# Kernel optimization log

Measured on AMD Instinct MI355X. Metric: run time of the kernel, lower is better.

The kernel has to match this reference:

```python
import jax, jax.numpy as jnp
import numpy as np

EPS = 1e-5
N_HEAD = 8
N_FREQS = 65
EMB_DIM = 128
E_DIM = 4            # ceil(256 / 65)
V_DIM = EMB_DIM // N_HEAD
CTX = 10


def prelu(x, a):
    return jnp.where(x >= 0, x, a * x)


def ln_last(x, g, b):
    # LayerNormalization4DCF_new: normalize over the fused (freq, chan) last axis
    mu = jnp.mean(x, axis=-1, keepdims=True)
    var = jnp.mean((x - mu) ** 2, axis=-1, keepdims=True)
    return (x - mu) / jnp.sqrt(var + EPS) * g + b


def head_proj(x, W, b, a, g, bt, H, Dh):
    # x: [B, T, F, C] -> [B*H, T, F*Dh], LayerNorm over last dim
    B, T, F, C = x.shape
    y = prelu(jnp.einsum('btfc,oc->btfo', x, W) + b, a)
    y = y.reshape(B, T, F, H, Dh).transpose(0, 3, 1, 2, 4).reshape(B * H, T, F * Dh)
    return ln_last(y, g, bt)


def setup_inputs() -> dict:
    key = jax.random.key(0)
    ks = jax.random.split(key, 8)
    B, T = 4, 500
    d = {}
    d['x'] = jax.random.normal(ks[0], (B, EMB_DIM, N_FREQS, T), dtype=jnp.float32)
    d['merged_context'] = jax.random.normal(ks[1], (B, EMB_DIM, N_FREQS, T), dtype=jnp.float32)
    d['K_buf'] = jnp.zeros((B * N_HEAD, CTX - 1, N_FREQS * E_DIM), dtype=jnp.float32)
    d['V_buf'] = jnp.zeros((B * N_HEAD, CTX - 1, N_FREQS * V_DIM), dtype=jnp.float32)
    d['W_Q'] = jax.random.normal(ks[2], (E_DIM * N_HEAD, EMB_DIM), dtype=jnp.float32) * 0.05
    d['b_Q'] = jnp.zeros((E_DIM * N_HEAD,), dtype=jnp.float32)
    d['a_Q'] = jnp.full((1,), 0.25, dtype=jnp.float32)
    d['g_Q'] = jnp.ones((N_FREQS * E_DIM,), dtype=jnp.float32)
    d['be_Q'] = jnp.zeros((N_FREQS * E_DIM,), dtype=jnp.float32)
    d['W_K'] = jax.random.normal(ks[3], (E_DIM * N_HEAD, EMB_DIM), dtype=jnp.float32) * 0.05
    d['b_K'] = jnp.zeros((E_DIM * N_HEAD,), dtype=jnp.float32)
    d['a_K'] = jnp.full((1,), 0.25, dtype=jnp.float32)
    d['g_K'] = jnp.ones((N_FREQS * E_DIM,), dtype=jnp.float32)
    d['be_K'] = jnp.zeros((N_FREQS * E_DIM,), dtype=jnp.float32)
    d['W_V'] = jax.random.normal(ks[4], (EMB_DIM, EMB_DIM), dtype=jnp.float32) * 0.05
    d['b_V'] = jnp.zeros((EMB_DIM,), dtype=jnp.float32)
    d['a_V'] = jnp.full((1,), 0.25, dtype=jnp.float32)
    d['g_V'] = jnp.ones((N_FREQS * V_DIM,), dtype=jnp.float32)
    d['be_V'] = jnp.zeros((N_FREQS * V_DIM,), dtype=jnp.float32)
    d['W_P'] = jax.random.normal(ks[5], (EMB_DIM, EMB_DIM), dtype=jnp.float32) * 0.05
    d['b_P'] = jnp.zeros((EMB_DIM,), dtype=jnp.float32)
    d['a_P'] = jnp.full((1,), 0.25, dtype=jnp.float32)
    d['g_P'] = jnp.ones((N_FREQS * EMB_DIM,), dtype=jnp.float32)
    d['be_P'] = jnp.zeros((N_FREQS * EMB_DIM,), dtype=jnp.float32)
    return d


def reference(x, merged_context, K_buf, V_buf,
              W_Q, b_Q, a_Q, g_Q, be_Q,
              W_K, b_K, a_K, g_K, be_K,
              W_V, b_V, a_V, g_V, be_V,
              W_P, b_P, a_P, g_P, be_P):
    # x, merged_context: [B, C, F, T] -> [B, T, F, C]
    xp = jnp.transpose(x, (0, 3, 2, 1))
    mc = jnp.transpose(merged_context, (0, 3, 2, 1))
    B, T, F, C = xp.shape
    H = N_HEAD

    Q = head_proj(xp, W_Q, b_Q, a_Q, g_Q, be_Q, H, E_DIM)     # [B*H, T, F*E]
    K = head_proj(mc, W_K, b_K, a_K, g_K, be_K, H, V_DIM * 0 + E_DIM)
    V = head_proj(mc, W_V, b_V, a_V, g_V, be_V, H, V_DIM)     # [B*H, T, F*Vd]

    Kfull = jnp.concatenate([K_buf, K], axis=1)               # [B*H, T+ctx-1, F*E]
    Vfull = jnp.concatenate([V_buf, V], axis=1)               # [B*H, T+ctx-1, F*Vd]
    K_buf_new = Kfull[:, -(CTX - 1):]
    V_buf_new = Vfull[:, -(CTX - 1):]

    # causal sliding windows of length ctx: [B*H, T, ctx, D]
    idx = jnp.arange(T)[:, None] + jnp.arange(CTX)[None, :]
    Kw = Kfull[:, idx, :]
    Vw = Vfull[:, idx, :]

    dqk = F * E_DIM
    scores = jnp.einsum('btd,btcd->btc', Q, Kw) / jnp.sqrt(jnp.float32(dqk))
    p = jax.nn.softmax(scores, axis=-1)                        # [B*H, T, ctx]
    Vo = jnp.einsum('btc,btcd->btd', p, Vw)                    # [B*H, T, F*Vd]

    # reassemble channels: [B*H, T, F*Vd] -> [B, T, F, H*Vd]
    z = Vo.reshape(B, H, T, F, V_DIM).transpose(0, 2, 3, 1, 4).reshape(B, T, F, H * V_DIM)

    y = prelu(jnp.einsum('btfc,oc->btfo', z, W_P) + b_P, a_P)  # [B, T, F, C]
    y = ln_last(y.reshape(B, T, F * C), g_P, be_P).reshape(B, T, F, C)

    out = y + xp
    out = jnp.transpose(out, (0, 3, 2, 1))                     # [B, C, F, T]
    return out, K_buf_new, V_buf_new
```

## Files before the change

### kernel.cpp

```cpp
#include <hip/hip_runtime.h>
#include <math.h>

#define NB   4
#define NT   500
#define NF   65
#define NC   128
#define NH   8
#define NE   4
#define NV   16
#define NCTX 10
#define DQ   260
#define DV   1040
#define DP   8320

#define MQ 0
#define RQ 16000
#define MK 32000
#define RK 48000
#define MV 64000
#define RV 80000

__global__ __launch_bounds__(256, 4) void proj32_k(const float* __restrict__ x,
    const float* __restrict__ W, const float* __restrict__ bias,
    const float* __restrict__ a, float* __restrict__ out,
    float* __restrict__ sS, float* __restrict__ sS2)
{
    __shared__ float Wl[NC * 32];
    int b = blockIdx.x / NF, f = blockIdx.x % NF;
    for (int idx = threadIdx.x; idx < 32 * NC; idx += 256) {
        int o = idx & 31, c = idx >> 5;
        Wl[c * 32 + o] = W[o * NC + c];
    }
    __syncthreads();
    int og = threadIdx.x >> 6;
    int tg = threadIdx.x & 63;
    int t0 = blockIdx.y * 256 + tg * 4;
    int t0c = t0 <= NT - 4 ? t0 : NT - 4;
    const float* xp = x + ((size_t)(b * NC) * NF + f) * NT + t0c;
    const float* wp = Wl + og * 8;
    const size_t xs = (size_t)NF * NT;
    float4 acc[8];
#pragma unroll
    for (int i = 0; i < 8; i++) acc[i] = make_float4(0.f, 0.f, 0.f, 0.f);
#pragma unroll 4
    for (int c = 0; c < NC; c++) {
        float4 xv = *(const float4*)(xp + (size_t)c * xs);
        const float* wc = wp + c * 32;
        float wv[8];
        *(float4*)(wv)     = *(const float4*)(wc);
        *(float4*)(wv + 4) = *(const float4*)(wc + 4);
#pragma unroll
        for (int i = 0; i < 8; i++) {
            acc[i].x += xv.x * wv[i];
            acc[i].y += xv.y * wv[i];
            acc[i].z += xv.z * wv[i];
            acc[i].w += xv.w * wv[i];
        }
    }
    if (t0 > NT - 4) return;
    float av = a[0];
#pragma unroll
    for (int i = 0; i < 8; i++) {
        int o = og * 8 + i;
        float bo = bias[o];
        float4 v = acc[i];
        v.x += bo; v.y += bo; v.z += bo; v.w += bo;
        v.x = v.x >= 0.f ? v.x : av * v.x;
        v.y = v.y >= 0.f ? v.y : av * v.y;
        v.z = v.z >= 0.f ? v.z : av * v.z;
        v.w = v.w >= 0.f ? v.w : av * v.w;
        acc[i] = v;
        int h = o >> 2, e = o & 3;
        *(float4*)(out + ((size_t)(b * NH + h) * DQ + f * NE + e) * NT + t0) = v;
    }
#pragma unroll
    for (int hh = 0; hh < 2; hh++) {
        int h = og * 2 + hh;
        float s0 = 0.f, s1 = 0.f, s2 = 0.f, s3 = 0.f;
        float q0 = 0.f, q1 = 0.f, q2 = 0.f, q3 = 0.f;
#pragma unroll
        for (int e = 0; e < 4; e++) {
            float4 v = acc[hh * 4 + e];
            s0 += v.x; s1 += v.y; s2 += v.z; s3 += v.w;
            q0 += v.x * v.x; q1 += v.y * v.y; q2 += v.z * v.z; q3 += v.w * v.w;
        }
        int base = (b * NH + h) * NT + t0;
        atomicAdd(&sS[base],     s0); atomicAdd(&sS[base + 1], s1);
        atomicAdd(&sS[base + 2], s2); atomicAdd(&sS[base + 3], s3);
        atomicAdd(&sS2[base],     q0); atomicAdd(&sS2[base + 1], q1);
        atomicAdd(&sS2[base + 2], q2); atomicAdd(&sS2[base + 3], q3);
    }
}

__global__ __launch_bounds__(256, 4) void projV_k(const float* __restrict__ x,
    const float* __restrict__ W, const float* __restrict__ bias,
    const float* __restrict__ a, float* __restrict__ out,
    float* __restrict__ sS, float* __restrict__ sS2)
{
    __shared__ float Wl[NC * 64];
    int b = blockIdx.x / NF, f = blockIdx.x % NF;
    int o0 = blockIdx.z * 64;
    for (int idx = threadIdx.x; idx < 64 * NC; idx += 256) {
        int o = idx & 63, c = idx >> 6;
        Wl[c * 64 + o] = W[(o0 + o) * NC + c];
    }
    __syncthreads();
    int og = threadIdx.x >> 6;
    int tg = threadIdx.x & 63;
    int t0 = blockIdx.y * 256 + tg * 4;
    int t0c = t0 <= NT - 4 ? t0 : NT - 4;
    const float* xp = x + ((size_t)(b * NC) * NF + f) * NT + t0c;
    const float* wp = Wl + og * 16;
    const size_t xs = (size_t)NF * NT;
    float4 acc[16];
#pragma unroll
    for (int i = 0; i < 16; i++) acc[i] = make_float4(0.f, 0.f, 0.f, 0.f);
#pragma unroll 2
    for (int c = 0; c < NC; c++) {
        float4 xv = *(const float4*)(xp + (size_t)c * xs);
        const float* wc = wp + c * 64;
        float wv[16];
        *(float4*)(wv)      = *(const float4*)(wc);
        *(float4*)(wv + 4)  = *(const float4*)(wc + 4);
        *(float4*)(wv + 8)  = *(const float4*)(wc + 8);
        *(float4*)(wv + 12) = *(const float4*)(wc + 12);
#pragma unroll
        for (int i = 0; i < 16; i++) {
            acc[i].x += xv.x * wv[i];
            acc[i].y += xv.y * wv[i];
            acc[i].z += xv.z * wv[i];
            acc[i].w += xv.w * wv[i];
        }
    }
    if (t0 > NT - 4) return;
    float av = a[0];
    int h = (o0 >> 4) + og;
    float s0 = 0.f, s1 = 0.f, s2 = 0.f, s3 = 0.f;
    float q0 = 0.f, q1 = 0.f, q2 = 0.f, q3 = 0.f;
#pragma unroll
    for (int i = 0; i < 16; i++) {
        int o = o0 + og * 16 + i;
        float bo = bias[o];
        float4 v = acc[i];
        v.x += bo; v.y += bo; v.z += bo; v.w += bo;
        v.x = v.x >= 0.f ? v.x : av * v.x;
        v.y = v.y >= 0.f ? v.y : av * v.y;
        v.z = v.z >= 0.f ? v.z : av * v.z;
        v.w = v.w >= 0.f ? v.w : av * v.w;
        *(float4*)(out + ((size_t)(b * NH + h) * DV + f * NV + i) * NT + t0) = v;
        s0 += v.x; s1 += v.y; s2 += v.z; s3 += v.w;
        q0 += v.x * v.x; q1 += v.y * v.y; q2 += v.z * v.z; q3 += v.w * v.w;
    }
    int base = (b * NH + h) * NT + t0;
    atomicAdd(&sS[base],     s0); atomicAdd(&sS[base + 1], s1);
    atomicAdd(&sS[base + 2], s2); atomicAdd(&sS[base + 3], s3);
    atomicAdd(&sS2[base],     q0); atomicAdd(&sS2[base + 1], q1);
    atomicAdd(&sS2[base + 2], q2); atomicAdd(&sS2[base + 3], q3);
}

__global__ __launch_bounds__(256, 4) void projP_k(const float* __restrict__ VoT,
    const float* __restrict__ W, const float* __restrict__ bias,
    const float* __restrict__ a, float* __restrict__ yraw,
    float* __restrict__ sP, float* __restrict__ s2P)
{
    __shared__ float Wl[NC * 64];
    int b = blockIdx.x / NF, f = blockIdx.x % NF;
    int o0 = blockIdx.z * 64;
    for (int idx = threadIdx.x; idx < 64 * NC; idx += 256) {
        int o = idx & 63, c = idx >> 6;
        Wl[c * 64 + o] = W[(o0 + o) * NC + c];
    }
    __syncthreads();
    int og = threadIdx.x >> 6;
    int tg = threadIdx.x & 63;
    int t0 = blockIdx.y * 256 + tg * 4;
    int t0c = t0 <= NT - 4 ? t0 : NT - 4;
    const float* zp = VoT + ((size_t)(b * NH) * DV + f * NV) * NT + t0c;
    const float* wp = Wl + og * 16;
    float4 acc[16];
#pragma unroll
    for (int i = 0; i < 16; i++) acc[i] = make_float4(0.f, 0.f, 0.f, 0.f);
    for (int hc = 0; hc < NH; hc++) {
        const float* zh = zp + (size_t)hc * DV * NT;
        const float* wh = wp + hc * 16 * 64;
#pragma unroll
        for (int v = 0; v < NV; v++) {
            float4 xv = *(const float4*)(zh + (size_t)v * NT);
            const float* wc = wh + v * 64;
            float wv[16];
            *(float4*)(wv)      = *(const float4*)(wc);
            *(float4*)(wv + 4)  = *(const float4*)(wc + 4);
            *(float4*)(wv + 8)  = *(const float4*)(wc + 8);
            *(float4*)(wv + 12) = *(const float4*)(wc + 12);
#pragma unroll
            for (int i = 0; i < 16; i++) {
                acc[i].x += xv.x * wv[i];
                acc[i].y += xv.y * wv[i];
                acc[i].z += xv.z * wv[i];
                acc[i].w += xv.w * wv[i];
            }
        }
    }
    if (t0 > NT - 4) return;
    float av = a[0];
    float s0 = 0.f, s1 = 0.f, s2 = 0.f, s3 = 0.f;
    float q0 = 0.f, q1 = 0.f, q2 = 0.f, q3 = 0.f;
#pragma unroll
    for (int i = 0; i < 16; i++) {
        int o = o0 + og * 16 + i;
        float bo = bias[o];
        float4 v = acc[i];
        v.x += bo; v.y += bo; v.z += bo; v.w += bo;
        v.x = v.x >= 0.f ? v.x : av * v.x;
        v.y = v.y >= 0.f ? v.y : av * v.y;
        v.z = v.z >= 0.f ? v.z : av * v.z;
        v.w = v.w >= 0.f ? v.w : av * v.w;
        *(float4*)(yraw + ((size_t)(b * NC + o) * NF + f) * NT + t0) = v;
        s0 += v.x; s1 += v.y; s2 += v.z; s3 += v.w;
        q0 += v.x * v.x; q1 += v.y * v.y; q2 += v.z * v.z; q3 += v.w * v.w;
    }
    int base = b * NT + t0;
    atomicAdd(&sP[base],     s0); atomicAdd(&sP[base + 1], s1);
    atomicAdd(&sP[base + 2], s2); atomicAdd(&sP[base + 3], s3);
    atomicAdd(&s2P[base],     q0); atomicAdd(&s2P[base + 1], q1);
    atomicAdd(&s2P[base + 2], q2); atomicAdd(&s2P[base + 3], q3);
}

__global__ __launch_bounds__(256) void finqkv_k(const float* __restrict__ stats,
    float* __restrict__ murs)
{
    int i = blockIdx.x * 256 + threadIdx.x;
    if (i >= 48000) return;
    int seg = i / 16000, j = i % 16000;
    float S = stats[seg * 32000 + j], S2 = stats[seg * 32000 + 16000 + j];
    float D = (seg < 2) ? 260.f : 1040.f;
    float mu = S / D;
    float var = S2 / D - mu * mu;
    murs[seg * 32000 + j] = mu;
    murs[seg * 32000 + 16000 + j] = rsqrtf(var + 1e-5f);
}

__global__ __launch_bounds__(256) void finp_k(const float* __restrict__ sP,
    const float* __restrict__ s2P, float* __restrict__ muP, float* __restrict__ rsP)
{
    int i = blockIdx.x * 256 + threadIdx.x;
    if (i >= NB * NT) return;
    float inv = 1.0f / (float)DP;
    float mu = sP[i] * inv;
    float var = s2P[i] * inv - mu * mu;
    muP[i] = mu;
    rsP[i] = rsqrtf(var + 1e-5f);
}

__global__ void copybuf_k(const float* __restrict__ Kt, const float* __restrict__ Vt,
    const float* __restrict__ murs,
    const float* __restrict__ g_K, const float* __restrict__ be_K,
    const float* __restrict__ g_V, const float* __restrict__ be_V,
    float* __restrict__ outK, float* __restrict__ outV)
{
    int i = blockIdx.x * 256 + threadIdx.x;
    const int NK = 32 * 9 * DQ;
    const int NVb = 32 * 9 * DV;
    if (i < NK) {
        int bh = i / (9 * DQ); int r = i % (9 * DQ); int j = r / DQ; int d = r % DQ;
        int tt = 491 + j;
        float v = Kt[(size_t)(bh * DQ + d) * NT + tt];
        float mu = murs[MK + bh * NT + tt], rs = murs[RK + bh * NT + tt];
        outK[i] = (v - mu) * rs * g_K[d] + be_K[d];
    } else if (i < NK + NVb) {
        int i2 = i - NK;
        int bh = i2 / (9 * DV); int r = i2 % (9 * DV); int j = r / DV; int d = r % DV;
        int tt = 491 + j;
        float v = Vt[(size_t)(bh * DV + d) * NT + tt];
        float mu = murs[MV + bh * NT + tt], rs = murs[RV + bh * NT + tt];
        outV[i2] = (v - mu) * rs * g_V[d] + be_V[d];
    }
}

__global__ __launch_bounds__(128) void scores_s1_k(const float* __restrict__ Qt,
    const float* __restrict__ Kt, const float* __restrict__ Kbuf,
    const float* __restrict__ murs,
    const float* __restrict__ g_Q, const float* __restrict__ be_Q,
    const float* __restrict__ g_K, const float* __restrict__ be_K,
    float* __restrict__ spart)
{
    int bh = blockIdx.x;
    int t = blockIdx.y * 128 + threadIdx.x;
    if (t >= NT) return;
    int z = blockIdx.z;
    int d0 = z * 13;
    float rsq = murs[RQ + bh * NT + t];
    float mq = -murs[MQ + bh * NT + t] * rsq;
    float s[NCTX];
    if (t >= NCTX - 1) {
        float rkc[NCTX], mkc[NCTX];
#pragma unroll
        for (int c = 0; c < NCTX; c++) {
            int tk = t - (NCTX - 1) + c;
            rkc[c] = murs[RK + bh * NT + tk];
            mkc[c] = -murs[MK + bh * NT + tk] * rkc[c];
        }
        float A[NCTX], SG = 0.f, SB = 0.f;
#pragma unroll
        for (int c = 0; c < NCTX; c++) A[c] = 0.f;
        const float* qp = Qt + ((size_t)bh * DQ + d0) * NT + t;
        const float* kp = Kt + ((size_t)bh * DQ + d0) * NT + (t - (NCTX - 1));
#pragma unroll 4
        for (int d = 0; d < 13; d++) {
            float gq = g_Q[d0 + d], bq = be_Q[d0 + d];
            float gk = g_K[d0 + d], bk = be_K[d0 + d];
            float qln = (qp[(size_t)d * NT] * rsq + mq) * gq + bq;
            float qg = qln * gk;
            SG += qg; SB += qln * bk;
            const float* kr = kp + (size_t)d * NT;
#pragma unroll
            for (int c = 0; c < NCTX; c++) A[c] += qg * kr[c];
        }
#pragma unroll
        for (int c = 0; c < NCTX; c++) s[c] = rkc[c] * A[c] + mkc[c] * SG + SB;
    } else {
#pragma unroll
        for (int c = 0; c < NCTX; c++) s[c] = 0.f;
        for (int d = 0; d < 13; d++) {
            float gq = g_Q[d0 + d], bq = be_Q[d0 + d];
            float gk = g_K[d0 + d], bk = be_K[d0 + d];
            float qln = (Qt[((size_t)bh * DQ + d0 + d) * NT + t] * rsq + mq) * gq + bq;
#pragma unroll
            for (int c = 0; c < NCTX; c++) {
                int tc = t + c;
                float kv;
                if (tc < NCTX - 1) {
                    kv = Kbuf[((size_t)bh * (NCTX - 1) + tc) * DQ + d0 + d];
                } else {
                    int tk = tc - (NCTX - 1);
                    float rk = murs[RK + bh * NT + tk];
                    float mk = murs[MK + bh * NT + tk];
                    kv = (Kt[((size_t)bh * DQ + d0 + d) * NT + tk] - mk) * rk * gk + bk;
                }
                s[c] += qln * kv;
            }
        }
    }
#pragma unroll
    for (int c = 0; c < NCTX; c++)
        spart[(size_t)((z * 32 + bh) * NCTX + c) * NT + t] = s[c];
}

__global__ __launch_bounds__(128) void softmax_k(const float* __restrict__ spart,
    float* __restrict__ p)
{
    int bh = blockIdx.x;
    int t = blockIdx.y * 128 + threadIdx.x;
    if (t >= NT) return;
    float s[NCTX];
#pragma unroll
    for (int c = 0; c < NCTX; c++) s[c] = 0.f;
    for (int z = 0; z < 20; z++) {
#pragma unroll
        for (int c = 0; c < NCTX; c++)
            s[c] += spart[(size_t)((z * 32 + bh) * NCTX + c) * NT + t];
    }
    const float sc = 0.06201736729460423f;
    float m = -1e30f;
#pragma unroll
    for (int c = 0; c < NCTX; c++) { s[c] *= sc; m = fmaxf(m, s[c]); }
    float den = 0.f;
#pragma unroll
    for (int c = 0; c < NCTX; c++) { s[c] = __expf(s[c] - m); den += s[c]; }
    float iden = 1.0f / den;
#pragma unroll
    for (int c = 0; c < NCTX; c++) p[(size_t)(bh * NCTX + c) * NT + t] = s[c] * iden;
}

__global__ __launch_bounds__(128) void vo_k(const float* __restrict__ p,
    const float* __restrict__ Vt, const float* __restrict__ Vbuf,
    const float* __restrict__ murs,
    const float* __restrict__ g_V, const float* __restrict__ be_V,
    float* __restrict__ VoT)
{
    int bh = blockIdx.x;
    int t = blockIdx.y * 128 + threadIdx.x;
    if (t >= NT) return;
    int d0 = blockIdx.z * 16;
    float pc[NCTX];
#pragma unroll
    for (int c = 0; c < NCTX; c++) pc[c] = p[(size_t)(bh * NCTX + c) * NT + t];
    if (t >= NCTX - 1) {
        float prs[NCTX], Cm = 0.f, Cp = 0.f;
#pragma unroll
        for (int c = 0; c < NCTX; c++) {
            int tv = t - (NCTX - 1) + c;
            float rs = murs[RV + bh * NT + tv];
            prs[c] = pc[c] * rs;
            Cm += pc[c] * (-murs[MV + bh * NT + tv] * rs);
            Cp += pc[c];
        }
        const float* vp = Vt + ((size_t)bh * DV + d0) * NT + (t - (NCTX - 1));
        float* op = VoT + ((size_t)bh * DV + d0) * NT + t;
#pragma unroll 4
        for (int d = 0; d < 16; d++) {
            float gv = g_V[d0 + d], bv = be_V[d0 + d];
            const float* vr = vp + (size_t)d * NT;
            float A = 0.f;
#pragma unroll
            for (int c = 0; c < NCTX; c++) A += prs[c] * vr[c];
            op[(size_t)d * NT] = gv * (A + Cm) + bv * Cp;
        }
    } else {
        for (int d = 0; d < 16; d++) {
            float gv = g_V[d0 + d], bv = be_V[d0 + d];
            float acc = 0.f;
#pragma unroll
            for (int c = 0; c < NCTX; c++) {
                int tc = t + c;
                float v;
                if (tc < NCTX - 1) {
                    v = Vbuf[((size_t)bh * (NCTX - 1) + tc) * DV + d0 + d];
                } else {
                    int tv = tc - (NCTX - 1);
                    float rs = murs[RV + bh * NT + tv];
                    float mu = murs[MV + bh * NT + tv];
                    v = (Vt[((size_t)bh * DV + d0 + d) * NT + tv] - mu) * rs * gv + bv;
                }
                acc += pc[c] * v;
            }
            VoT[((size_t)bh * DV + d0 + d) * NT + t] = acc;
        }
    }
}

__global__ __launch_bounds__(256) void lnp_apply(const float* __restrict__ yraw,
    const float* __restrict__ x, const float* __restrict__ g, const float* __restrict__ be,
    const float* __restrict__ muA, const float* __restrict__ rstdA, float* __restrict__ out)
{
    int bo = blockIdx.x; int b = bo >> 7, o = bo & 127;
    int t = blockIdx.y * 256 + threadIdx.x;
    if (t >= NT) return;
    float mu = muA[b * NT + t], rstd = rstdA[b * NT + t];
    for (int f = 0; f < NF; f++) {
        size_t idx = (size_t)((b * NC + o) * NF + f) * NT + t;
        int i = f * NC + o;
        float v = yraw[idx];
        out[idx] = (v - mu) * rstd * g[i] + be[i] + x[idx];
    }
}

extern "C" void kernel_launch(void* const* d_in, const int* in_sizes, int n_in,
                              void* d_out, int out_size, void* d_ws, size_t ws_size,
                              hipStream_t stream) {
    const float* x    = (const float*)d_in[0];
    const float* mc   = (const float*)d_in[1];
    const float* Kbuf = (const float*)d_in[2];
    const float* Vbuf = (const float*)d_in[3];
    const float* W_Q  = (const float*)d_in[4];
    const float* b_Q  = (const float*)d_in[5];
    const float* a_Q  = (const float*)d_in[6];
    const float* g_Q  = (const float*)d_in[7];
    const float* be_Q = (const float*)d_in[8];
    const float* W_K  = (const float*)d_in[9];
    const float* b_K  = (const float*)d_in[10];
    const float* a_K  = (const float*)d_in[11];
    const float* g_K  = (const float*)d_in[12];
    const float* be_K = (const float*)d_in[13];
    const float* W_V  = (const float*)d_in[14];
    const float* b_V  = (const float*)d_in[15];
    const float* a_V  = (const float*)d_in[16];
    const float* g_V  = (const float*)d_in[17];
    const float* be_V = (const float*)d_in[18];
    const float* W_P  = (const float*)d_in[19];
    const float* b_P  = (const float*)d_in[20];
    const float* a_P  = (const float*)d_in[21];
    const float* g_P  = (const float*)d_in[22];
    const float* be_P = (const float*)d_in[23];

    float* out  = (float*)d_out;
    float* outK = out + (size_t)NB * NC * NF * NT;
    float* outV = outK + 32 * 9 * DQ;

    float* stats = out;
    float* murs  = out + 96000;

    float* ws = (float*)d_ws;
    float* Qt   = ws;
    float* Kt   = Qt + (size_t)32 * DQ * NT;
    float* Vt   = Kt + (size_t)32 * DQ * NT;
    float* VoT  = Vt + (size_t)32 * DV * NT;
    float* pbuf = VoT + (size_t)32 * DV * NT;
    float* sP   = pbuf + (size_t)32 * NCTX * NT;
    float* s2P  = sP + NB * NT;
    float* muP  = s2P + NB * NT;
    float* rsP  = muP + NB * NT;
    float* yraw  = Vt;
    float* spart = VoT;

    dim3 blk(256);
    dim3 blk128(128);
    const int TCH = (NT + 255) / 256;
    const int TCH4 = (NT + 127) / 128;

    hipMemsetAsync(stats, 0, 96000 * sizeof(float), stream);
    hipMemsetAsync(sP, 0, 2 * NB * NT * sizeof(float), stream);

    proj32_k<<<dim3(NB * NF, 2), blk, 0, stream>>>(x,  W_Q, b_Q, a_Q, Qt,
                                                   stats + 0,     stats + 16000);
    proj32_k<<<dim3(NB * NF, 2), blk, 0, stream>>>(mc, W_K, b_K, a_K, Kt,
                                                   stats + 32000, stats + 48000);
    projV_k <<<dim3(NB * NF, 2, 2), blk, 0, stream>>>(mc, W_V, b_V, a_V, Vt,
                                                      stats + 64000, stats + 80000);

    finqkv_k<<<dim3(188), blk, 0, stream>>>(stats, murs);

    int nbuf = 32 * 9 * DQ + 32 * 9 * DV;
    copybuf_k<<<dim3((nbuf + 255) / 256), blk, 0, stream>>>(Kt, Vt, murs,
                                                            g_K, be_K, g_V, be_V, outK, outV);

    scores_s1_k<<<dim3(32, TCH4, 20), blk128, 0, stream>>>(Qt, Kt, Kbuf, murs,
                                                           g_Q, be_Q, g_K, be_K, spart);
    softmax_k  <<<dim3(32, TCH4), blk128, 0, stream>>>(spart, pbuf);
    vo_k       <<<dim3(32, TCH4, 65), blk128, 0, stream>>>(pbuf, Vt, Vbuf, murs,
                                                           g_V, be_V, VoT);

    projP_k<<<dim3(NB * NF, 2, 2), blk, 0, stream>>>(VoT, W_P, b_P, a_P, yraw, sP, s2P);

    finp_k<<<dim3((NB * NT + 255) / 256), blk, 0, stream>>>(sP, s2P, muP, rsP);

    lnp_apply<<<dim3(NB * NC, TCH), blk, 0, stream>>>(yraw, x, g_P, be_P, muP, rsP, out);
}
```

Baseline: 762.8 us.

## Retile projection kernels with LDS-staged input tiles and pre-transposed weights

```diff
diff --git a/kernel.cpp b/kernel.cpp
--- a/kernel.cpp
+++ b/kernel.cpp
@@ -20,70 +20,96 @@
 #define MV 64000
 #define RV 80000
 
-__global__ __launch_bounds__(256, 4) void proj32_k(const float* __restrict__ x,
-    const float* __restrict__ W, const float* __restrict__ bias,
+#define WTQ 0
+#define WTK 4096
+#define WTV 8192
+#define WTP 24576
+
+__global__ __launch_bounds__(256) void transW_k(const float* __restrict__ WQ,
+    const float* __restrict__ WK, const float* __restrict__ WV,
+    const float* __restrict__ WP, float* __restrict__ Wt)
+{
+    int i = blockIdx.x * 256 + threadIdx.x;
+    if (i < 4096) {
+        int c = i >> 5, o = i & 31;
+        Wt[WTQ + c * 32 + o] = WQ[o * 128 + c];
+    } else if (i < 8192) {
+        int j = i - 4096; int c = j >> 5, o = j & 31;
+        Wt[WTK + c * 32 + o] = WK[o * 128 + c];
+    } else if (i < 24576) {
+        int j = i - 8192; int c = j >> 7, o = j & 127;
+        Wt[WTV + c * 128 + o] = WV[o * 128 + c];
+    } else if (i < 40960) {
+        int j = i - 24576; int c = j >> 7, o = j & 127;
+        Wt[WTP + c * 128 + o] = WP[o * 128 + c];
+    }
+}
+
+__global__ __launch_bounds__(256, 2) void proj32_k(const float* __restrict__ x,
+    const float* __restrict__ Wt, const float* __restrict__ bias,
     const float* __restrict__ a, float* __restrict__ out,
     float* __restrict__ sS, float* __restrict__ sS2)
 {
-    __shared__ float Wl[NC * 32];
+    __shared__ float Xl[128 * 64];
+    __shared__ float Wl[128 * 32];
     int b = blockIdx.x / NF, f = blockIdx.x % NF;
-    for (int idx = threadIdx.x; idx < 32 * NC; idx += 256) {
-        int o = idx & 31, c = idx >> 5;
-        Wl[c * 32 + o] = W[o * NC + c];
+    int t0n = blockIdx.y * 64;
+    int t0c = t0n <= NT - 64 ? t0n : NT - 64;
+    int skipmin = t0n - t0c;
+    const size_t xs = (size_t)NF * NT;
+    const float* xb = x + (size_t)(b * NC) * xs + (size_t)f * NT + t0c;
+#pragma unroll
+    for (int k = 0; k < 8; k++) {
+        int q = threadIdx.x + k * 256;
+        int c = q >> 4, tc = (q & 15) * 4;
+        *(float4*)(Xl + q * 4) = *(const float4*)(xb + (size_t)c * xs + tc);
+    }
+#pragma unroll
+    for (int k = 0; k < 4; k++) {
+        int q = threadIdx.x + k * 256;
+        int c = q >> 3, col = (q & 7) * 4;
+        *(float4*)(Wl + q * 4) = *(const float4*)(Wt + c * 32 + col);
     }
     __syncthreads();
-    int og = threadIdx.x >> 6;
-    int tg = threadIdx.x & 63;
-    int t0 = blockIdx.y * 256 + tg * 4;
-    int t0c = t0 <= NT - 4 ? t0 : NT - 4;
-    const float* xp = x + ((size_t)(b * NC) * NF + f) * NT + t0c;
-    const float* wp = Wl + og * 8;
-    const size_t xs = (size_t)NF * NT;
-    float4 acc[8];
-#pragma unroll
-    for (int i = 0; i < 8; i++) acc[i] = make_float4(0.f, 0.f, 0.f, 0.f);
-#pragma unroll 4
+    int tt = threadIdx.x & 15;
+    int og = threadIdx.x >> 4;
+    float4 acc0 = make_float4(0.f, 0.f, 0.f, 0.f);
+    float4 acc1 = make_float4(0.f, 0.f, 0.f, 0.f);
+    const float* xr = Xl + tt * 4;
+    const float* wr = Wl + og * 2;
+#pragma unroll 8
     for (int c = 0; c < NC; c++) {
-        float4 xv = *(const float4*)(xp + (size_t)c * xs);
-        const float* wc = wp + c * 32;
-        float wv[8];
-        *(float4*)(wv)     = *(const float4*)(wc);
-        *(float4*)(wv + 4) = *(const float4*)(wc + 4);
-#pragma unroll
-        for (int i = 0; i < 8; i++) {
-            acc[i].x += xv.x * wv[i];
-            acc[i].y += xv.y * wv[i];
-            acc[i].z += xv.z * wv[i];
-            acc[i].w += xv.w * wv[i];
-        }
-    }
-    if (t0 > NT - 4) return;
+        float4 x4 = *(const float4*)(xr + c * 64);
+        float2 w2 = *(const float2*)(wr + c * 32);
+        acc0.x += w2.x * x4.x; acc0.y += w2.x * x4.y; acc0.z += w2.x * x4.z; acc0.w += w2.x * x4.w;
+        acc1.x += w2.y * x4.x; acc1.y += w2.y * x4.y; acc1.z += w2.y * x4.z; acc1.w += w2.y * x4.w;
+    }
+    if (tt * 4 < skipmin) return;
     float av = a[0];
-#pragma unroll
-    for (int i = 0; i < 8; i++) {
-        int o = og * 8 + i;
+    int t0 = t0c + tt * 4;
+    float s0 = 0.f, s1 = 0.f, s2 = 0.f, s3 = 0.f;
+    float q0 = 0.f, q1 = 0.f, q2 = 0.f, q3 = 0.f;
+#pragma unroll
+    for (int j = 0; j < 2; j++) {
+        int o = og * 2 + j;
         float bo = bias[o];
-        float4 v = acc[i];
+        float4 v = j == 0 ? acc0 : acc1;
         v.x += bo; v.y += bo; v.z += bo; v.w += bo;
         v.x = v.x >= 0.f ? v.x : av * v.x;
         v.y = v.y >= 0.f ? v.y : av * v.y;
         v.z = v.z >= 0.f ? v.z : av * v.z;
         v.w = v.w >= 0.f ? v.w : av * v.w;
-        acc[i] = v;
         int h = o >> 2, e = o & 3;
         *(float4*)(out + ((size_t)(b * NH + h) * DQ + f * NE + e) * NT + t0) = v;
-    }
-#pragma unroll
-    for (int hh = 0; hh < 2; hh++) {
-        int h = og * 2 + hh;
-        float s0 = 0.f, s1 = 0.f, s2 = 0.f, s3 = 0.f;
-        float q0 = 0.f, q1 = 0.f, q2 = 0.f, q3 = 0.f;
-#pragma unroll
-        for (int e = 0; e < 4; e++) {
-            float4 v = acc[hh * 4 + e];
-            s0 += v.x; s1 += v.y; s2 += v.z; s3 += v.w;
-            q0 += v.x * v.x; q1 += v.y * v.y; q2 += v.z * v.z; q3 += v.w * v.w;
-        }
+        s0 += v.x; s1 += v.y; s2 += v.z; s3 += v.w;
+        q0 += v.x * v.x; q1 += v.y * v.y; q2 += v.z * v.z; q3 += v.w * v.w;
+    }
+    s0 += __shfl_xor(s0, 16); s1 += __shfl_xor(s1, 16);
+    s2 += __shfl_xor(s2, 16); s3 += __shfl_xor(s3, 16);
+    q0 += __shfl_xor(q0, 16); q1 += __shfl_xor(q1, 16);
+    q2 += __shfl_xor(q2, 16); q3 += __shfl_xor(q3, 16);
+    if ((threadIdx.x & 16) == 0) {
+        int h = og >> 1;
         int base = (b * NH + h) * NT + t0;
         atomicAdd(&sS[base],     s0); atomicAdd(&sS[base + 1], s1);
         atomicAdd(&sS[base + 2], s2); atomicAdd(&sS[base + 3], s3);
@@ -92,124 +118,143 @@
     }
 }
 
-__global__ __launch_bounds__(256, 4) void projV_k(const float* __restrict__ x,
-    const float* __restrict__ W, const float* __restrict__ bias,
+__global__ __launch_bounds__(256, 2) void projV_k(const float* __restrict__ x,
+    const float* __restrict__ Wt, const float* __restrict__ bias,
     const float* __restrict__ a, float* __restrict__ out,
     float* __restrict__ sS, float* __restrict__ sS2)
 {
-    __shared__ float Wl[NC * 64];
+    __shared__ float Xl[128 * 64];
+    __shared__ float Wl[128 * 64];
     int b = blockIdx.x / NF, f = blockIdx.x % NF;
-    int o0 = blockIdx.z * 64;
-    for (int idx = threadIdx.x; idx < 64 * NC; idx += 256) {
-        int o = idx & 63, c = idx >> 6;
-        Wl[c * 64 + o] = W[(o0 + o) * NC + c];
+    int oc = blockIdx.z * 64;
+    int t0n = blockIdx.y * 64;
+    int t0c = t0n <= NT - 64 ? t0n : NT - 64;
+    int skipmin = t0n - t0c;
+    const size_t xs = (size_t)NF * NT;
+    const float* xb = x + (size_t)(b * NC) * xs + (size_t)f * NT + t0c;
+    const float* wb = Wt + oc;
+#pragma unroll
+    for (int k = 0; k < 8; k++) {
+        int q = threadIdx.x + k * 256;
+        int c = q >> 4, tc = (q & 15) * 4;
+        *(float4*)(Xl + q * 4) = *(const float4*)(xb + (size_t)c * xs + tc);
+    }
+#pragma unroll
+    for (int k = 0; k < 8; k++) {
+        int q = threadIdx.x + k * 256;
+        int c = q >> 4, col = (q & 15) * 4;
+        *(float4*)(Wl + q * 4) = *(const float4*)(wb + c * 128 + col);
     }
     __syncthreads();
-    int og = threadIdx.x >> 6;
-    int tg = threadIdx.x & 63;
-    int t0 = blockIdx.y * 256 + tg * 4;
-    int t0c = t0 <= NT - 4 ? t0 : NT - 4;
-    const float* xp = x + ((size_t)(b * NC) * NF + f) * NT + t0c;
-    const float* wp = Wl + og * 16;
-    const size_t xs = (size_t)NF * NT;
-    float4 acc[16];
-#pragma unroll
-    for (int i = 0; i < 16; i++) acc[i] = make_float4(0.f, 0.f, 0.f, 0.f);
-#pragma unroll 2
+    int tt = threadIdx.x & 15;
+    int og = threadIdx.x >> 4;
+    float4 acc0 = make_float4(0.f, 0.f, 0.f, 0.f);
+    float4 acc1 = make_float4(0.f, 0.f, 0.f, 0.f);
+    float4 acc2 = make_float4(0.f, 0.f, 0.f, 0.f);
+    float4 acc3 = make_float4(0.f, 0.f, 0.f, 0.f);
+    const float* xr = Xl + tt * 4;
+    const float* wr = Wl + og * 4;
+#pragma unroll 8
     for (int c = 0; c < NC; c++) {
-        float4 xv = *(const float4*)(xp + (size_t)c * xs);
-        const float* wc = wp + c * 64;
-        float wv[16];
-        *(float4*)(wv)      = *(const float4*)(wc);
-        *(float4*)(wv + 4)  = *(const float4*)(wc + 4);
-        *(float4*)(wv + 8)  = *(const float4*)(wc + 8);
-        *(float4*)(wv + 12) = *(const float4*)(wc + 12);
-#pragma unroll
-        for (int i = 0; i < 16; i++) {
-            acc[i].x += xv.x * wv[i];
-            acc[i].y += xv.y * wv[i];
-            acc[i].z += xv.z * wv[i];
-            acc[i].w += xv.w * wv[i];
-        }
-    }
-    if (t0 > NT - 4) return;
+        float4 x4 = *(const float4*)(xr + c * 64);
+        float4 w4 = *(const float4*)(wr + c * 64);
+        acc0.x += w4.x * x4.x; acc0.y += w4.x * x4.y; acc0.z += w4.x * x4.z; acc0.w += w4.x * x4.w;
+        acc1.x += w4.y * x4.x; acc1.y += w4.y * x4.y; acc1.z += w4.y * x4.z; acc1.w += w4.y * x4.w;
+        acc2.x += w4.z * x4.x; acc2.y += w4.z * x4.y; acc2.z += w4.z * x4.z; acc2.w += w4.z * x4.w;
+        acc3.x += w4.w * x4.x; acc3.y += w4.w * x4.y; acc3.z += w4.w * x4.z; acc3.w += w4.w * x4.w;
+    }
+    if (tt * 4 < skipmin) return;
     float av = a[0];
-    int h = (o0 >> 4) + og;
+    int t0 = t0c + tt * 4;
+    int h = (oc + og * 4) >> 4;
     float s0 = 0.f, s1 = 0.f, s2 = 0.f, s3 = 0.f;
     float q0 = 0.f, q1 = 0.f, q2 = 0.f, q3 = 0.f;
 #pragma unroll
-    for (int i = 0; i < 16; i++) {
-        int o = o0 + og * 16 + i;
+    for (int j = 0; j < 4; j++) {
+        int o = oc + og * 4 + j;
         float bo = bias[o];
-        float4 v = acc[i];
+        float4 v = j == 0 ? acc0 : j == 1 ? acc1 : j == 2 ? acc2 : acc3;
         v.x += bo; v.y += bo; v.z += bo; v.w += bo;
         v.x = v.x >= 0.f ? v.x : av * v.x;
         v.y = v.y >= 0.f ? v.y : av * v.y;
         v.z = v.z >= 0.f ? v.z : av * v.z;
         v.w = v.w >= 0.f ? v.w : av * v.w;
-        *(float4*)(out + ((size_t)(b * NH + h) * DV + f * NV + i) * NT + t0) = v;
+        *(float4*)(out + ((size_t)(b * NH + h) * DV + f * NV + (o & 15)) * NT + t0) = v;
         s0 += v.x; s1 += v.y; s2 += v.z; s3 += v.w;
         q0 += v.x * v.x; q1 += v.y * v.y; q2 += v.z * v.z; q3 += v.w * v.w;
     }
-    int base = (b * NH + h) * NT + t0;
-    atomicAdd(&sS[base],     s0); atomicAdd(&sS[base + 1], s1);
-    atomicAdd(&sS[base + 2], s2); atomicAdd(&sS[base + 3], s3);
-    atomicAdd(&sS2[base],     q0); atomicAdd(&sS2[base + 1], q1);
-    atomicAdd(&sS2[base + 2], q2); atomicAdd(&sS2[base + 3], q3);
-}
-
-__global__ __launch_bounds__(256, 4) void projP_k(const float* __restrict__ VoT,
-    const float* __restrict__ W, const float* __restrict__ bias,
+    s0 += __shfl_xor(s0, 16); s1 += __shfl_xor(s1, 16);
+    s2 += __shfl_xor(s2, 16); s3 += __shfl_xor(s3, 16);
+    q0 += __shfl_xor(q0, 16); q1 += __shfl_xor(q1, 16);
+    q2 += __shfl_xor(q2, 16); q3 += __shfl_xor(q3, 16);
+    s0 += __shfl_xor(s0, 32); s1 += __shfl_xor(s1, 32);
+    s2 += __shfl_xor(s2, 32); s3 += __shfl_xor(s3, 32);
+    q0 += __shfl_xor(q0, 32); q1 += __shfl_xor(q1, 32);
+    q2 += __shfl_xor(q2, 32); q3 += __shfl_xor(q3, 32);
+    if ((threadIdx.x & 48) == 0) {
+        int base = (b * NH + h) * NT + t0;
+        atomicAdd(&sS[base],     s0); atomicAdd(&sS[base + 1], s1);
+        atomicAdd(&sS[base + 2], s2); atomicAdd(&sS[base + 3], s3);
+        atomicAdd(&sS2[base],     q0); atomicAdd(&sS2[base + 1], q1);
+        atomicAdd(&sS2[base + 2], q2); atomicAdd(&sS2[base + 3], q3);
+    }
+}
+
+__global__ __launch_bounds__(256, 2) void projP_k(const float* __restrict__ VoT,
+    const float* __restrict__ Wt, const float* __restrict__ bias,
     const float* __restrict__ a, float* __restrict__ yraw,
     float* __restrict__ sP, float* __restrict__ s2P)
 {
-    __shared__ float Wl[NC * 64];
+    __shared__ float Xl[128 * 64];
+    __shared__ float Wl[128 * 64];
     int b = blockIdx.x / NF, f = blockIdx.x % NF;
-    int o0 = blockIdx.z * 64;
-    for (int idx = threadIdx.x; idx < 64 * NC; idx += 256) {
-        int o = idx & 63, c = idx >> 6;
-        Wl[c * 64 + o] = W[(o0 + o) * NC + c];
+    int oc = blockIdx.z * 64;
+    int t0n = blockIdx.y * 64;
+    int t0c = t0n <= NT - 64 ? t0n : NT - 64;
+    int skipmin = t0n - t0c;
+    const float* zb = VoT + ((size_t)(b * NH) * DV + f * NV) * NT + t0c;
+    const float* wb = Wt + oc;
+#pragma unroll
+    for (int k = 0; k < 8; k++) {
+        int q = threadIdx.x + k * 256;
+        int r = q >> 4, tc = (q & 15) * 4;
+        const float* src = zb + ((size_t)(r >> 4) * DV + (r & 15)) * NT + tc;
+        *(float4*)(Xl + q * 4) = *(const float4*)src;
+    }
+#pragma unroll
+    for (int k = 0; k < 8; k++) {
+        int q = threadIdx.x + k * 256;
+        int c = q >> 4, col = (q & 15) * 4;
+        *(float4*)(Wl + q * 4) = *(const float4*)(wb + c * 128 + col);
     }
     __syncthreads();
-    int og = threadIdx.x >> 6;
-    int tg = threadIdx.x & 63;
-    int t0 = blockIdx.y * 256 + tg * 4;
-    int t0c = t0 <= NT - 4 ? t0 : NT - 4;
-    const float* zp = VoT + ((size_t)(b * NH) * DV + f * NV) * NT + t0c;
-    const float* wp = Wl + og * 16;
-    float4 acc[16];
-#pragma unroll
-    for (int i = 0; i < 16; i++) acc[i] = make_float4(0.f, 0.f, 0.f, 0.f);
-    for (int hc = 0; hc < NH; hc++) {
-        const float* zh = zp + (size_t)hc * DV * NT;
-        const float* wh = wp + hc * 16 * 64;
-#pragma unroll
-        for (int v = 0; v < NV; v++) {
-            float4 xv = *(const float4*)(zh + (size_t)v * NT);
-            const float* wc = wh + v * 64;
-            float wv[16];
-            *(float4*)(wv)      = *(const float4*)(wc);
-            *(float4*)(wv + 4)  = *(const float4*)(wc + 4);
-            *(float4*)(wv + 8)  = *(const float4*)(wc + 8);
-            *(float4*)(wv + 12) = *(const float4*)(wc + 12);
-#pragma unroll
-            for (int i = 0; i < 16; i++) {
-                acc[i].x += xv.x * wv[i];
-                acc[i].y += xv.y * wv[i];
-                acc[i].z += xv.z * wv[i];
-                acc[i].w += xv.w * wv[i];
-            }
-        }
-    }
-    if (t0 > NT - 4) return;
+    int tt = threadIdx.x & 15;
+    int og = threadIdx.x >> 4;
+    float4 acc0 = make_float4(0.f, 0.f, 0.f, 0.f);
+    float4 acc1 = make_float4(0.f, 0.f, 0.f, 0.f);
+    float4 acc2 = make_float4(0.f, 0.f, 0.f, 0.f);
+    float4 acc3 = make_float4(0.f, 0.f, 0.f, 0.f);
+    const float* xr = Xl + tt * 4;
+    const float* wr = Wl + og * 4;
+#pragma unroll 8
+    for (int c = 0; c < NC; c++) {
+        float4 x4 = *(const float4*)(xr + c * 64);
+        float4 w4 = *(const float4*)(wr + c * 64);
+        acc0.x += w4.x * x4.x; acc0.y += w4.x * x4.y; acc0.z += w4.x * x4.z; acc0.w += w4.x * x4.w;
+        acc1.x += w4.y * x4.x; acc1.y += w4.y * x4.y; acc1.z += w4.y * x4.z; acc1.w += w4.y * x4.w;
+        acc2.x += w4.z * x4.x; acc2.y += w4.z * x4.y; acc2.z += w4.z * x4.z; acc2.w += w4.z * x4.w;
+        acc3.x += w4.w * x4.x; acc3.y += w4.w * x4.y; acc3.z += w4.w * x4.z; acc3.w += w4.w * x4.w;
+    }
+    if (tt * 4 < skipmin) return;
     float av = a[0];
+    int t0 = t0c + tt * 4;
     float s0 = 0.f, s1 = 0.f, s2 = 0.f, s3 = 0.f;
     float q0 = 0.f, q1 = 0.f, q2 = 0.f, q3 = 0.f;
 #pragma unroll
-    for (int i = 0; i < 16; i++) {
-        int o = o0 + og * 16 + i;
+    for (int j = 0; j < 4; j++) {
+        int o = oc + og * 4 + j;
         float bo = bias[o];
-        float4 v = acc[i];
+        float4 v = j == 0 ? acc0 : j == 1 ? acc1 : j == 2 ? acc2 : acc3;
         v.x += bo; v.y += bo; v.z += bo; v.w += bo;
         v.x = v.x >= 0.f ? v.x : av * v.x;
         v.y = v.y >= 0.f ? v.y : av * v.y;
@@ -219,11 +264,21 @@
         s0 += v.x; s1 += v.y; s2 += v.z; s3 += v.w;
         q0 += v.x * v.x; q1 += v.y * v.y; q2 += v.z * v.z; q3 += v.w * v.w;
     }
-    int base = b * NT + t0;
-    atomicAdd(&sP[base],     s0); atomicAdd(&sP[base + 1], s1);
-    atomicAdd(&sP[base + 2], s2); atomicAdd(&sP[base + 3], s3);
-    atomicAdd(&s2P[base],     q0); atomicAdd(&s2P[base + 1], q1);
-    atomicAdd(&s2P[base + 2], q2); atomicAdd(&s2P[base + 3], q3);
+    s0 += __shfl_xor(s0, 16); s1 += __shfl_xor(s1, 16);
+    s2 += __shfl_xor(s2, 16); s3 += __shfl_xor(s3, 16);
+    q0 += __shfl_xor(q0, 16); q1 += __shfl_xor(q1, 16);
+    q2 += __shfl_xor(q2, 16); q3 += __shfl_xor(q3, 16);
+    s0 += __shfl_xor(s0, 32); s1 += __shfl_xor(s1, 32);
+    s2 += __shfl_xor(s2, 32); s3 += __shfl_xor(s3, 32);
+    q0 += __shfl_xor(q0, 32); q1 += __shfl_xor(q1, 32);
+    q2 += __shfl_xor(q2, 32); q3 += __shfl_xor(q3, 32);
+    if ((threadIdx.x & 48) == 0) {
+        int base = b * NT + t0;
+        atomicAdd(&sP[base],     s0); atomicAdd(&sP[base + 1], s1);
+        atomicAdd(&sP[base + 2], s2); atomicAdd(&sP[base + 3], s3);
+        atomicAdd(&s2P[base],     q0); atomicAdd(&s2P[base + 1], q1);
+        atomicAdd(&s2P[base + 2], q2); atomicAdd(&s2P[base + 3], q3);
+    }
 }
 
 __global__ __launch_bounds__(256) void finqkv_k(const float* __restrict__ stats,
@@ -490,6 +545,7 @@
     float* s2P  = sP + NB * NT;
     float* muP  = s2P + NB * NT;
     float* rsP  = muP + NB * NT;
+    float* Wt   = rsP + NB * NT;
     float* yraw  = Vt;
     float* spart = VoT;
 
@@ -501,11 +557,13 @@
     hipMemsetAsync(stats, 0, 96000 * sizeof(float), stream);
     hipMemsetAsync(sP, 0, 2 * NB * NT * sizeof(float), stream);
 
-    proj32_k<<<dim3(NB * NF, 2), blk, 0, stream>>>(x,  W_Q, b_Q, a_Q, Qt,
+    transW_k<<<dim3(160), blk, 0, stream>>>(W_Q, W_K, W_V, W_P, Wt);
+
+    proj32_k<<<dim3(NB * NF, 8), blk, 0, stream>>>(x,  Wt + WTQ, b_Q, a_Q, Qt,
                                                    stats + 0,     stats + 16000);
-    proj32_k<<<dim3(NB * NF, 2), blk, 0, stream>>>(mc, W_K, b_K, a_K, Kt,
+    proj32_k<<<dim3(NB * NF, 8), blk, 0, stream>>>(mc, Wt + WTK, b_K, a_K, Kt,
                                                    stats + 32000, stats + 48000);
-    projV_k <<<dim3(NB * NF, 2, 2), blk, 0, stream>>>(mc, W_V, b_V, a_V, Vt,
+    projV_k <<<dim3(NB * NF, 8, 2), blk, 0, stream>>>(mc, Wt + WTV, b_V, a_V, Vt,
                                                       stats + 64000, stats + 80000);
 
     finqkv_k<<<dim3(188), blk, 0, stream>>>(stats, murs);
@@ -520,7 +578,7 @@
     vo_k       <<<dim3(32, TCH4, 65), blk128, 0, stream>>>(pbuf, Vt, Vbuf, murs,
                                                            g_V, be_V, VoT);
 
-    projP_k<<<dim3(NB * NF, 2, 2), blk, 0, stream>>>(VoT, W_P, b_P, a_P, yraw, sP, s2P);
+    projP_k<<<dim3(NB * NF, 8, 2), blk, 0, stream>>>(VoT, Wt + WTP, b_P, a_P, yraw, sP, s2P);
 
     finp_k<<<dim3((NB * NT + 255) / 256), blk, 0, stream>>>(sP, s2P, muP, rsP);
 
```

After: 793.5 us. +4.0%, slower.
